# Optimization experiments

Measured on AMD Instinct MI355X. Metric: run time of the kernel, lower is better.

Reference implementation:

```python
import jax, jax.numpy as jnp
import numpy as np

B, N1, N2, C2, K = 8, 2048, 128, 256, 3
D_POS, H0, H1 = 32, 512, 1024


def setup_inputs() -> dict:
    key = jax.random.key(0)
    ks = jax.random.split(key, 14)
    return {
        "xyz1": jax.random.normal(ks[0], (B, N1, 3), jnp.float32),
        "xyz2": jax.random.normal(ks[1], (B, N2, 3), jnp.float32),
        "feat2": jax.random.normal(ks[2], (B, N2, C2), jnp.float32),
        "lrf2": jax.random.normal(ks[3], (B, N2, 3, 3), jnp.float32),
        "w_pos": jax.random.normal(ks[4], (D_POS, 4), jnp.float32) * 0.1,
        "pos_scale": jax.random.uniform(ks[5], (D_POS,), jnp.float32, 0.5, 1.5),
        "pos_bias": jax.random.normal(ks[6], (D_POS,), jnp.float32) * 0.1,
        "w0": jax.random.normal(ks[7], (H0, C2 + D_POS), jnp.float32) * 0.05,
        "s0": jax.random.uniform(ks[8], (H0,), jnp.float32, 0.5, 1.5),
        "b0": jax.random.normal(ks[9], (H0,), jnp.float32) * 0.1,
        "w1": jax.random.normal(ks[10], (H1, H0), jnp.float32) * 0.04,
        "s1": jax.random.uniform(ks[11], (H1,), jnp.float32, 0.5, 1.5),
        "b1": jax.random.normal(ks[12], (H1,), jnp.float32) * 0.1,
        "k": K,
    }


def reference(xyz1, xyz2, feat2, lrf2, w_pos, pos_scale, pos_bias,
              w0, s0, b0, w1, s1, b1, k):
    Bb = xyz1.shape[0]
    # --- get_dists: full pairwise sqrt-distance matrix (B, N1, N2) ---
    d2 = (jnp.sum(xyz1 * xyz1, -1)[:, :, None]
          + jnp.sum(xyz2 * xyz2, -1)[:, None, :]
          - 2.0 * jnp.einsum('bmc,bnc->bmn', xyz1, xyz2))
    dists = jnp.sqrt(jnp.where(d2 < 0, 1e-7, d2))
    # --- k-NN: smallest k in ascending order (== torch.sort then slice) ---
    _, inds = jax.lax.top_k(-dists, k)                    # (B, N1, k)
    bidx = jnp.arange(Bb)[:, None, None]
    feat_nb = feat2[bidx, inds]                           # (B, N1, k, C2)
    close = xyz2[bidx, inds]                              # (B, N1, k, 3)
    lrf_nb = lrf2[bidx, inds]                             # (B, N1, k, 3, 3)
    # --- geometric angle embedding ---
    rel = xyz1[:, :, None, :] - close                     # (B, N1, k, 3)
    rel_norm = jnp.linalg.norm(rel, axis=-1)              # (B, N1, k)
    unit = rel / jnp.maximum(rel_norm, 1e-12)[..., None]  # F.normalize eps
    angle = jnp.einsum('bnkij,bnkj->bnki', lrf_nb, unit)  # (B, N1, k, 3)
    rp = jnp.concatenate([rel_norm[..., None], angle], -1)  # (B, N1, k, 4)
    # --- posembed: 1x1 Conv2d (no bias) + folded BN + LeakyReLU(0.2) ---
    pos = jax.nn.leaky_relu(
        jnp.einsum('bnkc,oc->bnko', rp, w_pos) * pos_scale + pos_bias, 0.2)
    # --- backbone: two 1x1 convs with folded BN + ReLU ---
    x = jnp.concatenate([feat_nb, pos], -1)               # (B, N1, k, C2+32)
    h0 = jax.nn.relu(jnp.einsum('bnkc,oc->bnko', x, w0) * s0 + b0)
    h1 = jax.nn.relu(jnp.einsum('bnkc,oc->bnko', h0, w1) * s1 + b1)
    # --- sum over neighbors, return (B, C_out, N1) like torch ---
    return jnp.transpose(jnp.sum(h1, axis=2), (0, 2, 1))
```

## Files before the change

### kernel.cpp

```cpp
#include <hip/hip_runtime.h>


typedef unsigned short u16;
typedef __bf16 bf16x8 __attribute__((ext_vector_type(8)));
typedef float f32x4 __attribute__((ext_vector_type(4)));
typedef u16 u16x4 __attribute__((ext_vector_type(4)));
typedef u16 u16x8 __attribute__((ext_vector_type(8)));

#define BQ 8
#define N1Q 2048
#define N2Q 128
#define C2Q 256
#define DPOS 32
#define H0Q 512
#define H1Q 1024
#define NQ (BQ * N1Q)

#define WS_W0P 262144u
#define WS_W1 294912u
#define WS_F 1867776u
#define WS_H0 3964928u
#define WS_POS 54296576u
#define WS_IDX 57442304u

__device__ __forceinline__ u16 f2bf(float f) {
  unsigned int u = __builtin_bit_cast(unsigned int, f);
  return (u16)((u + 0x7FFFu + ((u >> 16) & 1u)) >> 16);
}

__device__ __forceinline__ void load16_lds(const void* g, void* l) {
  __builtin_amdgcn_global_load_lds(
      (const __attribute__((address_space(1))) unsigned int*)g,
      (__attribute__((address_space(3))) unsigned int*)l, 16, 0, 0);
}

__global__ __launch_bounds__(512, 2) void prep(
    const float* __restrict__ xyz1, const float* __restrict__ xyz2,
    const float* __restrict__ lrf2, const float* __restrict__ w_pos,
    const float* __restrict__ pscale, const float* __restrict__ pbias,
    const float* __restrict__ w0, const float* __restrict__ w1,
    const float* __restrict__ feat2,
    u16* __restrict__ posw, int* __restrict__ idxw,
    u16* __restrict__ w0p, u16* __restrict__ w1b, float* __restrict__ F) {
  const int t = threadIdx.x;

  if (blockIdx.x >= 392) {
    const int wv = t >> 6, lane = t & 63;
    const int quad = lane >> 4, cc = lane & 15;
    const int wid = (blockIdx.x - 392) * 8 + wv;
    const int m0 = (wid >> 5) * 16;
    const int n0 = (wid & 31) * 16;
    const float* fa0 = feat2 + (size_t)(m0 + cc) * 256 + quad * 8;
    const float* fb0 = w0 + (size_t)(n0 + cc) * 288 + quad * 8;
    f32x4 acc = {};
#pragma unroll
    for (int q8 = 0; q8 < 8; q8++) {
      u16x8 au, bu;
#pragma unroll
      for (int e = 0; e < 8; e++) {
        au[e] = f2bf(fa0[q8 * 32 + e]);
        bu[e] = f2bf(fb0[q8 * 32 + e]);
      }
      acc = __builtin_amdgcn_mfma_f32_16x16x32_bf16(
          __builtin_bit_cast(bf16x8, au), __builtin_bit_cast(bf16x8, bu), acc,
          0, 0, 0);
    }
#pragma unroll
    for (int r = 0; r < 4; r++)
      F[(size_t)(m0 + quad * 4 + r) * H0Q + n0 + cc] = acc[r];
    return;
  }

  if (blockIdx.x >= 128) {
    int j = (blockIdx.x - 128) * 512 + t;
    if (j < 131072) {
      f32x4 v = *(const f32x4*)(w1 + (size_t)j * 4);
      u16x4 o = {f2bf(v[0]), f2bf(v[1]), f2bf(v[2]), f2bf(v[3])};
      *(u16x4*)(w1b + (size_t)j * 4) = o;
    } else {
      int k = j - 131072;
      int h = k >> 3, c4 = k & 7;
      f32x4 v = *(const f32x4*)(w0 + h * 288 + 256 + c4 * 4);
      u16x4 o = {f2bf(v[0]), f2bf(v[1]), f2bf(v[2]), f2bf(v[3])};
      *(u16x4*)(w0p + h * 32 + c4 * 4) = o;
    }
    return;
  }

  __shared__ float xyz2s[N2Q * 3];
  __shared__ float n2s[N2Q];
  __shared__ float lrfs[N2Q * 9];
  __shared__ float wps[DPOS * 4];
  __shared__ float pss[DPOS];
  __shared__ float pbs[DPOS];
  __shared__ float candd[128 * 13];
  __shared__ int candi[128 * 13];
  __shared__ int idxb[384];

  const int qb = blockIdx.x * 128;
  const int b = qb >> 11;

  for (int i = t; i < N2Q * 3; i += 512) xyz2s[i] = xyz2[b * N2Q * 3 + i];
  for (int i = t; i < N2Q * 9; i += 512) lrfs[i] = lrf2[b * N2Q * 9 + i];
  if (t < DPOS * 4) wps[t] = w_pos[t];
  if (t < DPOS) { pss[t] = pscale[t]; pbs[t] = pbias[t]; }
  __syncthreads();
  if (t < N2Q) {
    float x = xyz2s[t * 3], y = xyz2s[t * 3 + 1], z = xyz2s[t * 3 + 2];
    n2s[t] = x * x + y * y + z * z;
  }
  __syncthreads();

  {
    const int ql = t >> 2, qt = t & 3;
    const int q = qb + ql;
    const float px = xyz1[q * 3], py = xyz1[q * 3 + 1], pz = xyz1[q * 3 + 2];
    const float pn = px * px + py * py + pz * pz;
    float d0 = 1e30f, d1 = 1e30f, d2v = 1e30f;
    int i0 = 0, i1 = 0, i2 = 0;
    const int ibeg = qt * 32;
    for (int i = ibeg; i < ibeg + 32; i++) {
      float dt = px * xyz2s[i * 3] + py * xyz2s[i * 3 + 1] + pz * xyz2s[i * 3 + 2];
      float d = pn + n2s[i] - 2.f * dt;
      if (d < d0) {
        d2v = d1; i2 = i1; d1 = d0; i1 = i0; d0 = d; i0 = i;
      } else if (d < d1) {
        d2v = d1; i2 = i1; d1 = d; i1 = i;
      } else if (d < d2v) {
        d2v = d; i2 = i;
      }
    }
    int base = ql * 13 + qt * 3;
    candd[base] = d0;      candi[base] = i0;
    candd[base + 1] = d1;  candi[base + 1] = i1;
    candd[base + 2] = d2v; candi[base + 2] = i2;
  }
  __syncthreads();

  if (t < 128) {
    float d0 = 1e30f, d1 = 1e30f, d2v = 1e30f;
    int i0 = 0, i1 = 0, i2 = 0;
    int base = t * 13;
#pragma unroll
    for (int c = 0; c < 12; c++) {
      float d = candd[base + c];
      int id = candi[base + c];
      if (d < d0) {
        d2v = d1; i2 = i1; d1 = d0; i1 = i0; d0 = d; i0 = id;
      } else if (d < d1) {
        d2v = d1; i2 = i1; d1 = d; i1 = id;
      } else if (d < d2v) {
        d2v = d; i2 = id;
      }
    }
    idxb[t] = i0;
    idxb[128 + t] = i1;
    idxb[256 + t] = i2;
  }
  __syncthreads();

  if (t < 384) {
    const int j = t >> 7, ql = t & 127;
    const int q = qb + ql;
    const float px = xyz1[q * 3], py = xyz1[q * 3 + 1], pz = xyz1[q * 3 + 2];
    const int id = idxb[j * 128 + ql];
    float rx = px - xyz2s[id * 3];
    float ry = py - xyz2s[id * 3 + 1];
    float rz = pz - xyz2s[id * 3 + 2];
    float rn = sqrtf(rx * rx + ry * ry + rz * rz);
    float inv = 1.f / fmaxf(rn, 1e-12f);
    float ux = rx * inv, uy = ry * inv, uz = rz * inv;
    const float* L = lrfs + id * 9;
    float a0 = L[0] * ux + L[1] * uy + L[2] * uz;
    float a1 = L[3] * ux + L[4] * uy + L[5] * uz;
    float a2 = L[6] * ux + L[7] * uy + L[8] * uz;
    const size_t row = (size_t)j * NQ + q;
    idxw[row] = id;
#pragma unroll
    for (int c = 0; c < 4; c++) {
      u16x8 chunk;
#pragma unroll
      for (int e = 0; e < 8; e++) {
        int o = c * 8 + e;
        float v = wps[o * 4] * rn + wps[o * 4 + 1] * a0 + wps[o * 4 + 2] * a1 +
                  wps[o * 4 + 3] * a2;
        v = v * pss[o] + pbs[o];
        v = (v >= 0.f) ? v : 0.2f * v;
        chunk[e] = f2bf(v);
      }
      *(u16x8*)(posw + row * 32 + c * 8) = chunk;
    }
  }
}

__global__ __launch_bounds__(256, 4) void h0_kernel(
    const u16* __restrict__ posw, const int* __restrict__ idxw,
    const u16* __restrict__ w0p, const float* __restrict__ F,
    const float* __restrict__ s0, const float* __restrict__ b0,
    u16* __restrict__ H0) {
  const int t = threadIdx.x;
  const int wv = t >> 6, lane = t & 63;
  const int quad = lane >> 4, cc = lane & 15;
  const int r0 = (blockIdx.x * 4 + wv) * 16;

  const int r = r0 + cc;
  const int q = r & (NQ - 1);
  const int bb = q >> 11;
  const int idv = idxw[r];
  const float* Fr = F + ((size_t)(bb * N2Q + idv)) * H0Q;
  u16* Hr = H0 + (size_t)r * H0Q;

  const bf16x8 afr = *(const bf16x8*)(posw + (size_t)r * 32 + quad * 8);
  const f32x4 zf = {};

#pragma unroll 4
  for (int nt = 0; nt < 32; nt++) {
    const bf16x8 bfr = *(const bf16x8*)(w0p + (nt * 16 + cc) * 32 + quad * 8);
    f32x4 acc = __builtin_amdgcn_mfma_f32_16x16x32_bf16(bfr, afr, zf, 0, 0, 0);
    const int hb = nt * 16 + quad * 4;
    const f32x4 sv = *(const f32x4*)(s0 + hb);
    const f32x4 bv = *(const f32x4*)(b0 + hb);
    const f32x4 fv = *(const f32x4*)(Fr + hb);
    u16x4 o4;
#pragma unroll
    for (int e = 0; e < 4; e++) {
      float h = (fv[e] + acc[e]) * sv[e] + bv[e];
      h = h > 0.f ? h : 0.f;
      o4[e] = f2bf(h);
    }
    *(u16x4*)(Hr + hb) = o4;
  }
}

__global__ __launch_bounds__(512, 2) void gemm2(const u16* __restrict__ A,
                                                const u16* __restrict__ W,
                                                const float* __restrict__ s,
                                                const float* __restrict__ bz,
                                                float* __restrict__ out) {
  __shared__ alignas(16) char smem[3][40960];
  const int id = blockIdx.x;
  const int xcd = id & 7, g = id >> 3;
  const int m0 = (xcd * 16 + (g >> 2)) * 128;
  const int n0 = (g & 3) * 256;
  const int t = threadIdx.x;
  const int wv = t >> 6, lane = t & 63;
  const int wm = wv >> 2, wn = wv & 3;
  const int quad = lane >> 4, cc = lane & 15;
  const int lr = lane & 15, lk = quad * 8;

  const size_t aOff = (size_t)(m0 + wv * 16 + lr) * 512 + lk;
  size_t bOff[2];
#pragma unroll
  for (int i = 0; i < 2; i++)
    bOff[i] = (size_t)(n0 + (wv * 2 + i) * 16 + lr) * 512 + lk;

  auto stage = [&](int kt, int buf) {
    const int k0 = kt << 5;
    char* dst = smem[buf] + (lane << 4);
#pragma unroll
    for (int j = 0; j < 3; j++)
      load16_lds(A + (size_t)j * NQ * H0Q + aOff + k0,
                 dst + j * 8192 + wv * 1024);
#pragma unroll
    for (int i = 0; i < 2; i++)
      load16_lds(W + bOff[i] + k0, dst + 24576 + (wv * 2 + i) * 1024);
  };

  f32x4 acc[3][4][4] = {};

  stage(0, 0);
  stage(1, 1);

  int bi = 0, sb = 2;
  for (int kt = 0; kt < 16; kt++) {
    if (kt < 15)
      asm volatile("s_waitcnt vmcnt(5)" ::: "memory");
    else
      asm volatile("s_waitcnt vmcnt(0)" ::: "memory");
    __builtin_amdgcn_s_barrier();
    if (kt + 2 < 16) {
      stage(kt + 2, sb);
      sb = (sb == 2) ? 0 : sb + 1;
    }
    const char* base = smem[bi] + (lane << 4);
    bf16x8 bf[4];
#pragma unroll
    for (int nt = 0; nt < 4; nt++)
      bf[nt] = *(const bf16x8*)(base + 24576 + (wn * 4 + nt) * 1024);
#pragma unroll
    for (int j = 0; j < 3; j++) {
      bf16x8 af[4];
#pragma unroll
      for (int mt = 0; mt < 4; mt++)
        af[mt] = *(const bf16x8*)(base + j * 8192 + (wm * 4 + mt) * 1024);
      __builtin_amdgcn_s_setprio(1);
#pragma unroll
      for (int mt = 0; mt < 4; mt++)
#pragma unroll
        for (int nt = 0; nt < 4; nt++)
          acc[j][mt][nt] = __builtin_amdgcn_mfma_f32_16x16x32_bf16(
              af[mt], bf[nt], acc[j][mt][nt], 0, 0, 0);
      __builtin_amdgcn_s_setprio(0);
    }
    bi = (bi == 2) ? 0 : bi + 1;
  }

#pragma unroll
  for (int nt = 0; nt < 4; nt++) {
    int gn = n0 + wn * 64 + nt * 16 + cc;
    float sv = s[gn], bv = bz[gn];
#pragma unroll
    for (int mt = 0; mt < 4; mt++) {
      int gm = m0 + wm * 64 + mt * 16 + quad * 4;
#pragma unroll
      for (int r = 0; r < 4; r++) {
        float h0v = acc[0][mt][nt][r] * sv + bv;
        float h1v = acc[1][mt][nt][r] * sv + bv;
        float h2v = acc[2][mt][nt][r] * sv + bv;
        float v = (h0v > 0.f ? h0v : 0.f) + (h1v > 0.f ? h1v : 0.f) +
                  (h2v > 0.f ? h2v : 0.f);
        int q = gm + r;
        out[((size_t)(q >> 11) * H1Q + gn) * N1Q + (q & 2047)] = v;
      }
    }
  }
}

extern "C" void kernel_launch(void* const* d_in, const int* in_sizes, int n_in,
                              void* d_out, int out_size, void* d_ws,
                              size_t ws_size, hipStream_t stream) {
  const float* xyz1 = (const float*)d_in[0];
  const float* xyz2 = (const float*)d_in[1];
  const float* feat2 = (const float*)d_in[2];
  const float* lrf2 = (const float*)d_in[3];
  const float* w_pos = (const float*)d_in[4];
  const float* pscale = (const float*)d_in[5];
  const float* pbias = (const float*)d_in[6];
  const float* w0 = (const float*)d_in[7];
  const float* s0 = (const float*)d_in[8];
  const float* b0 = (const float*)d_in[9];
  const float* w1 = (const float*)d_in[10];
  const float* s1 = (const float*)d_in[11];
  const float* b1 = (const float*)d_in[12];
  float* out = (float*)d_out;

  char* ws = (char*)d_ws;
  u16* w0p = (u16*)(ws + WS_W0P);
  u16* w1b = (u16*)(ws + WS_W1);
  float* F = (float*)(ws + WS_F);
  u16* H0 = (u16*)(ws + WS_H0);
  u16* posw = (u16*)(ws + WS_POS);
  int* idxw = (int*)(ws + WS_IDX);

  prep<<<648, 512, 0, stream>>>(xyz1, xyz2, lrf2, w_pos, pscale, pbias, w0,
                                w1, feat2, posw, idxw, w0p, w1b, F);
  h0_kernel<<<768, 256, 0, stream>>>(posw, idxw, w0p, F, s0, b0, H0);
  gemm2<<<512, 512, 0, stream>>>(H0, w1b, s1, b1, out);
}
```

Measured before the change: 196.6 us.

## Fuse kNN/pos-embed prep with H0 layer into one kernel using LDS-resident F

Merges the prep and h0 kernels into a single fused_pre kernel. Each kNN block recomputes its batch's feat2·W0 product into shared memory, one half of H0 at a time. It then computes the first layer directly from LDS-held positional embeddings and neighbour indices. This removes the global round trips for F, posw, idxw and the packed w0 slice, plus one kernel launch. In exchange, every block in a batch redundantly recomputes F. The heavy H0 write is now done by only 128 blocks with large LDS use, which limits occupancy and CU coverage.

```diff
diff --git a/kernel.cpp b/kernel.cpp
--- a/kernel.cpp
+++ b/kernel.cpp
@@ -16,12 +16,10 @@
 #define H1Q 1024
 #define NQ (BQ * N1Q)
 
-#define WS_W0P 262144u
 #define WS_W1 294912u
-#define WS_F 1867776u
 #define WS_H0 3964928u
-#define WS_POS 54296576u
-#define WS_IDX 57442304u
+
+#define FB_STRIDE 260
 
 __device__ __forceinline__ u16 f2bf(float f) {
   unsigned int u = __builtin_bit_cast(unsigned int, f);
@@ -34,69 +32,48 @@
       (__attribute__((address_space(3))) unsigned int*)l, 16, 0, 0);
 }
 
-__global__ __launch_bounds__(512, 2) void prep(
+__device__ __forceinline__ bf16x8 cvt8(const float* p) {
+  f32x4 a = *(const f32x4*)p;
+  f32x4 b = *(const f32x4*)(p + 4);
+  u16x8 o = {f2bf(a[0]), f2bf(a[1]), f2bf(a[2]), f2bf(a[3]),
+             f2bf(b[0]), f2bf(b[1]), f2bf(b[2]), f2bf(b[3])};
+  return __builtin_bit_cast(bf16x8, o);
+}
+
+__global__ __launch_bounds__(512, 2) void fused_pre(
     const float* __restrict__ xyz1, const float* __restrict__ xyz2,
     const float* __restrict__ lrf2, const float* __restrict__ w_pos,
     const float* __restrict__ pscale, const float* __restrict__ pbias,
     const float* __restrict__ w0, const float* __restrict__ w1,
-    const float* __restrict__ feat2,
-    u16* __restrict__ posw, int* __restrict__ idxw,
-    u16* __restrict__ w0p, u16* __restrict__ w1b, float* __restrict__ F) {
+    const float* __restrict__ feat2, const float* __restrict__ s0,
+    const float* __restrict__ b0, u16* __restrict__ w1b,
+    u16* __restrict__ H0) {
   const int t = threadIdx.x;
 
-  if (blockIdx.x >= 392) {
-    const int wv = t >> 6, lane = t & 63;
-    const int quad = lane >> 4, cc = lane & 15;
-    const int wid = (blockIdx.x - 392) * 8 + wv;
-    const int m0 = (wid >> 5) * 16;
-    const int n0 = (wid & 31) * 16;
-    const float* fa0 = feat2 + (size_t)(m0 + cc) * 256 + quad * 8;
-    const float* fb0 = w0 + (size_t)(n0 + cc) * 288 + quad * 8;
-    f32x4 acc = {};
-#pragma unroll
-    for (int q8 = 0; q8 < 8; q8++) {
-      u16x8 au, bu;
-#pragma unroll
-      for (int e = 0; e < 8; e++) {
-        au[e] = f2bf(fa0[q8 * 32 + e]);
-        bu[e] = f2bf(fb0[q8 * 32 + e]);
-      }
-      acc = __builtin_amdgcn_mfma_f32_16x16x32_bf16(
-          __builtin_bit_cast(bf16x8, au), __builtin_bit_cast(bf16x8, bu), acc,
-          0, 0, 0);
-    }
-#pragma unroll
-    for (int r = 0; r < 4; r++)
-      F[(size_t)(m0 + quad * 4 + r) * H0Q + n0 + cc] = acc[r];
+  if (blockIdx.x >= 128) {
+    int j = (int)(blockIdx.x - 128) * 512 + t;
+    f32x4 v = *(const f32x4*)(w1 + (size_t)j * 4);
+    u16x4 o = {f2bf(v[0]), f2bf(v[1]), f2bf(v[2]), f2bf(v[3])};
+    *(u16x4*)(w1b + (size_t)j * 4) = o;
     return;
   }
 
-  if (blockIdx.x >= 128) {
-    int j = (blockIdx.x - 128) * 512 + t;
-    if (j < 131072) {
-      f32x4 v = *(const f32x4*)(w1 + (size_t)j * 4);
-      u16x4 o = {f2bf(v[0]), f2bf(v[1]), f2bf(v[2]), f2bf(v[3])};
-      *(u16x4*)(w1b + (size_t)j * 4) = o;
-    } else {
-      int k = j - 131072;
-      int h = k >> 3, c4 = k & 7;
-      f32x4 v = *(const f32x4*)(w0 + h * 288 + 256 + c4 * 4);
-      u16x4 o = {f2bf(v[0]), f2bf(v[1]), f2bf(v[2]), f2bf(v[3])};
-      *(u16x4*)(w0p + h * 32 + c4 * 4) = o;
-    }
-    return;
-  }
-
-  __shared__ float xyz2s[N2Q * 3];
-  __shared__ float n2s[N2Q];
-  __shared__ float lrfs[N2Q * 9];
-  __shared__ float wps[DPOS * 4];
-  __shared__ float pss[DPOS];
-  __shared__ float pbs[DPOS];
-  __shared__ float candd[128 * 13];
-  __shared__ int candi[128 * 13];
+  __shared__ alignas(16) char smem[133120];
   __shared__ int idxb[384];
-
+  __shared__ alignas(16) u16 posl[384 * 32];
+
+  float* const xyz2s = (float*)smem;
+  float* const n2s = xyz2s + 384;
+  float* const lrfs = n2s + 128;
+  float* const wps = lrfs + 1152;
+  float* const pss = wps + 128;
+  float* const pbs = pss + 32;
+  float* const candd = pbs + 32;
+  int* const candi = (int*)(candd + 1664);
+  float* const Fb = (float*)smem;
+
+  const int wv = t >> 6, lane = t & 63;
+  const int quad = lane >> 4, cc = lane & 15;
   const int qb = blockIdx.x * 128;
   const int b = qb >> 11;
 
@@ -160,10 +137,10 @@
   __syncthreads();
 
   if (t < 384) {
-    const int j = t >> 7, ql = t & 127;
+    const int ql = t & 127;
     const int q = qb + ql;
     const float px = xyz1[q * 3], py = xyz1[q * 3 + 1], pz = xyz1[q * 3 + 2];
-    const int id = idxb[j * 128 + ql];
+    const int id = idxb[t];
     float rx = px - xyz2s[id * 3];
     float ry = py - xyz2s[id * 3 + 1];
     float rz = pz - xyz2s[id * 3 + 2];
@@ -174,8 +151,7 @@
     float a0 = L[0] * ux + L[1] * uy + L[2] * uz;
     float a1 = L[3] * ux + L[4] * uy + L[5] * uz;
     float a2 = L[6] * ux + L[7] * uy + L[8] * uz;
-    const size_t row = (size_t)j * NQ + q;
-    idxw[row] = id;
+    u16* pd = posl + t * 32;
 #pragma unroll
     for (int c = 0; c < 4; c++) {
       u16x8 chunk;
@@ -188,47 +164,78 @@
         v = (v >= 0.f) ? v : 0.2f * v;
         chunk[e] = f2bf(v);
       }
-      *(u16x8*)(posw + row * 32 + c * 8) = chunk;
-    }
-  }
-}
-
-__global__ __launch_bounds__(256, 4) void h0_kernel(
-    const u16* __restrict__ posw, const int* __restrict__ idxw,
-    const u16* __restrict__ w0p, const float* __restrict__ F,
-    const float* __restrict__ s0, const float* __restrict__ b0,
-    u16* __restrict__ H0) {
-  const int t = threadIdx.x;
-  const int wv = t >> 6, lane = t & 63;
-  const int quad = lane >> 4, cc = lane & 15;
-  const int r0 = (blockIdx.x * 4 + wv) * 16;
-
-  const int r = r0 + cc;
-  const int q = r & (NQ - 1);
-  const int bb = q >> 11;
-  const int idv = idxw[r];
-  const float* Fr = F + ((size_t)(bb * N2Q + idv)) * H0Q;
-  u16* Hr = H0 + (size_t)r * H0Q;
-
-  const bf16x8 afr = *(const bf16x8*)(posw + (size_t)r * 32 + quad * 8);
-  const f32x4 zf = {};
-
-#pragma unroll 4
-  for (int nt = 0; nt < 32; nt++) {
-    const bf16x8 bfr = *(const bf16x8*)(w0p + (nt * 16 + cc) * 32 + quad * 8);
-    f32x4 acc = __builtin_amdgcn_mfma_f32_16x16x32_bf16(bfr, afr, zf, 0, 0, 0);
-    const int hb = nt * 16 + quad * 4;
-    const f32x4 sv = *(const f32x4*)(s0 + hb);
-    const f32x4 bv = *(const f32x4*)(b0 + hb);
-    const f32x4 fv = *(const f32x4*)(Fr + hb);
-    u16x4 o4;
-#pragma unroll
-    for (int e = 0; e < 4; e++) {
-      float h = (fv[e] + acc[e]) * sv[e] + bv[e];
-      h = h > 0.f ? h : 0.f;
-      o4[e] = f2bf(h);
-    }
-    *(u16x4*)(Hr + hb) = o4;
+      *(u16x8*)(pd + c * 8) = chunk;
+    }
+  }
+  __syncthreads();
+
+  for (int half = 0; half < 2; half++) {
+    {
+      const int hbase = half * 256 + wv * 32;
+      f32x4 acc[8][2] = {};
+      for (int k0 = 0; k0 < 256; k0 += 32) {
+        bf16x8 bf[2];
+#pragma unroll
+        for (int nt = 0; nt < 2; nt++)
+          bf[nt] = cvt8(w0 + (size_t)(hbase + nt * 16 + cc) * 288 + k0 +
+                        quad * 8);
+#pragma unroll
+        for (int mt = 0; mt < 8; mt++) {
+          bf16x8 af = cvt8(feat2 + (size_t)(b * N2Q + mt * 16 + cc) * 256 +
+                           k0 + quad * 8);
+#pragma unroll
+          for (int nt = 0; nt < 2; nt++)
+            acc[mt][nt] = __builtin_amdgcn_mfma_f32_16x16x32_bf16(
+                af, bf[nt], acc[mt][nt], 0, 0, 0);
+        }
+      }
+#pragma unroll
+      for (int mt = 0; mt < 8; mt++)
+#pragma unroll
+        for (int nt = 0; nt < 2; nt++)
+#pragma unroll
+          for (int r = 0; r < 4; r++)
+            Fb[(mt * 16 + quad * 4 + r) * FB_STRIDE + wv * 32 + nt * 16 + cc] =
+                acc[mt][nt][r];
+    }
+    __syncthreads();
+
+    {
+      int idv[3], rowg[3];
+      bf16x8 afr[3];
+#pragma unroll
+      for (int mt = 0; mt < 3; mt++) {
+        int rl = wv * 48 + mt * 16 + cc;
+        idv[mt] = idxb[rl];
+        rowg[mt] = (rl >> 7) * NQ + qb + (rl & 127);
+        afr[mt] = *(const bf16x8*)(posl + rl * 32 + quad * 8);
+      }
+      const f32x4 zf = {};
+#pragma unroll 2
+      for (int nt = 0; nt < 16; nt++) {
+        const int hglob = half * 256 + nt * 16 + cc;
+        bf16x8 bfr = cvt8(w0 + (size_t)hglob * 288 + 256 + quad * 8);
+        const int hb4 = half * 256 + nt * 16 + quad * 4;
+        const f32x4 sv = *(const f32x4*)(s0 + hb4);
+        const f32x4 bv = *(const f32x4*)(b0 + hb4);
+#pragma unroll
+        for (int mt = 0; mt < 3; mt++) {
+          f32x4 aq = __builtin_amdgcn_mfma_f32_16x16x32_bf16(bfr, afr[mt], zf,
+                                                             0, 0, 0);
+          f32x4 fv = *(const f32x4*)(Fb + idv[mt] * FB_STRIDE + nt * 16 +
+                                     quad * 4);
+          u16x4 o4;
+#pragma unroll
+          for (int e = 0; e < 4; e++) {
+            float h = (fv[e] + aq[e]) * sv[e] + bv[e];
+            h = h > 0.f ? h : 0.f;
+            o4[e] = f2bf(h);
+          }
+          *(u16x4*)(H0 + (size_t)rowg[mt] * H0Q + hb4) = o4;
+        }
+      }
+    }
+    __syncthreads();
   }
 }
 
@@ -345,15 +352,10 @@
   float* out = (float*)d_out;
 
   char* ws = (char*)d_ws;
-  u16* w0p = (u16*)(ws + WS_W0P);
   u16* w1b = (u16*)(ws + WS_W1);
-  float* F = (float*)(ws + WS_F);
   u16* H0 = (u16*)(ws + WS_H0);
-  u16* posw = (u16*)(ws + WS_POS);
-  int* idxw = (int*)(ws + WS_IDX);
-
-  prep<<<648, 512, 0, stream>>>(xyz1, xyz2, lrf2, w_pos, pscale, pbias, w0,
-                                w1, feat2, posw, idxw, w0p, w1b, F);
-  h0_kernel<<<768, 256, 0, stream>>>(posw, idxw, w0p, F, s0, b0, H0);
+
+  fused_pre<<<384, 512, 0, stream>>>(xyz1, xyz2, lrf2, w_pos, pscale, pbias,
+                                     w0, w1, feat2, s0, b0, w1b, H0);
   gemm2<<<512, 512, 0, stream>>>(H0, w1b, s1, b1, out);
 }
```

After: 268.1 us. 1.36x slower.
